# Optimization experiments

Hardware: AMD Instinct MI355X
Metric: run time of the kernel (lower is better)

Reference implementation:

```python
import jax, jax.numpy as jnp
import numpy as np

B, T, I, H, V = 32, 64, 512, 512, 32000


def setup_inputs() -> dict:
    key = jax.random.key(0)
    ks = jax.random.split(key, 8)
    s_in = 1.0 / np.sqrt(H)  # torch LSTMCell/Linear uniform init scale
    return {
        "isequence": jax.random.normal(ks[0], (B, T, I), dtype=jnp.float32),
        "hidden_t": jax.random.normal(ks[1], (B, H), dtype=jnp.float32),
        "W_ih": jax.random.uniform(ks[2], (4 * H, I), jnp.float32, -s_in, s_in),
        "W_hh": jax.random.uniform(ks[3], (4 * H, H), jnp.float32, -s_in, s_in),
        "b_ih": jax.random.uniform(ks[4], (4 * H,), jnp.float32, -s_in, s_in),
        "b_hh": jax.random.uniform(ks[5], (4 * H,), jnp.float32, -s_in, s_in),
        "W_out": jax.random.uniform(ks[6], (V, H), jnp.float32, -s_in, s_in),
        "b_out": jax.random.uniform(ks[7], (V,), jnp.float32, -s_in, s_in),
    }


def reference(isequence, hidden_t, W_ih, W_hh, b_ih, b_hh, W_out, b_out):
    # isequence: [B, T, I] -> time-major [T, B, I] (matches permute(1,0,2))
    xs = jnp.transpose(isequence, (1, 0, 2))
    # Precompute input-to-gate projections for all timesteps: [T, B, 4H]
    x_gates = jnp.einsum("tbi,gi->tbg", xs, W_ih) + b_ih + b_hh
    c0 = jnp.zeros_like(hidden_t)  # init_hidden zeros cell state

    def step(carry, xg):
        h, c = carry
        gates = xg + h @ W_hh.T  # [B, 4H], torch gate order: i, f, g, o
        i_g, f_g, g_g, o_g = jnp.split(gates, 4, axis=-1)
        i_g = jax.nn.sigmoid(i_g)
        f_g = jax.nn.sigmoid(f_g)
        g_g = jnp.tanh(g_g)
        o_g = jax.nn.sigmoid(o_g)
        c_new = f_g * c + i_g * g_g
        h_new = o_g * jnp.tanh(c_new)
        logits = h_new @ W_out.T + b_out  # [B, V]
        return (h_new, c_new), logits

    _, osequence = jax.lax.scan(step, (hidden_t, c0), x_gates)  # [T, B, V]
    return jnp.transpose(osequence, (1, 0, 2))  # [B, T, V]
```

## Files before the change

kernel.cpp:

```cpp
#include <hip/hip_runtime.h>
#include <hip/hip_bf16.h>

typedef unsigned short u16;
typedef unsigned int u32;
typedef __attribute__((ext_vector_type(4))) float f32x4;
typedef __attribute__((ext_vector_type(8))) short short8;
typedef __attribute__((ext_vector_type(4))) unsigned short u16x4;
typedef __attribute__((ext_vector_type(4))) unsigned int u32x4;

#define LSTM_NBLK 16

static __device__ __forceinline__ u16 f2bf(float f) {
  union { float f; unsigned u; } v; v.f = f;
  unsigned r = v.u + 0x7FFFu + ((v.u >> 16) & 1u);
  return (u16)(r >> 16);
}

static __device__ __forceinline__ void gload_lds16(const void* g, void* l) {
  __builtin_amdgcn_global_load_lds(
      (const __attribute__((address_space(1))) unsigned int*)g,
      (__attribute__((address_space(3))) unsigned int*)l, 16, 0, 0);
}

static __device__ __forceinline__ short8 ld_b128_sc(const void* p) {
  short8 r;
  asm volatile("global_load_dwordx4 %0, %1, off sc0 sc1"
               : "=v"(r) : "v"(p) : "memory");
  return r;
}
static __device__ __forceinline__ unsigned ld_u32_sc_wait(const unsigned* p) {
  unsigned r;
  asm volatile("global_load_dword %0, %1, off sc0 sc1\n\ts_waitcnt vmcnt(0)"
               : "=v"(r) : "v"(p) : "memory");
  return r;
}
static __device__ __forceinline__ void st_u32_sc(void* p, unsigned v) {
  asm volatile("global_store_dword %0, %1, off sc0 sc1"
               :: "v"(p), "v"(v) : "memory");
}
static __device__ __forceinline__ void waitcnt0() {
  asm volatile("s_waitcnt vmcnt(0)" ::: "memory");
  __builtin_amdgcn_sched_barrier(0);
}

__global__ void prep_kernel(const float* __restrict__ iseq, const float* __restrict__ h0,
                            const float* __restrict__ wih, const float* __restrict__ whh,
                            const float* __restrict__ wout,
                            u16* __restrict__ wout_bf, u16* __restrict__ wih_bf,
                            u16* __restrict__ whh_bf, u16* __restrict__ ax,
                            u32* __restrict__ h2u, unsigned* __restrict__ flags) {
  const int S0 = 4096000;
  const int S1 = S0 + 262144;
  const int S2 = S1 + 262144;
  const int S3 = S2 + 262144;
  const int S4 = S3 + 8192;
  const int S5 = S4 + 256;
  int u = blockIdx.x * blockDim.x + threadIdx.x;
  int stride = gridDim.x * blockDim.x;
  for (; u < S5; u += stride) {
    if (u < S0) {
      int e = u * 4; f32x4 v = *(const f32x4*)(wout + e);
      u16x4 o; o[0]=f2bf(v[0]); o[1]=f2bf(v[1]); o[2]=f2bf(v[2]); o[3]=f2bf(v[3]);
      *(u16x4*)(wout_bf + e) = o;
    } else if (u < S1) {
      int e = (u - S0) * 4; f32x4 v = *(const f32x4*)(wih + e);
      u16x4 o; o[0]=f2bf(v[0]); o[1]=f2bf(v[1]); o[2]=f2bf(v[2]); o[3]=f2bf(v[3]);
      *(u16x4*)(wih_bf + e) = o;
    } else if (u < S2) {
      int e = (u - S1) * 4; f32x4 v = *(const f32x4*)(whh + e);
      u16x4 o; o[0]=f2bf(v[0]); o[1]=f2bf(v[1]); o[2]=f2bf(v[2]); o[3]=f2bf(v[3]);
      *(u16x4*)(whh_bf + e) = o;
    } else if (u < S3) {
      int e = (u - S2) * 4; int m = e >> 9; int k = e & 511;
      int b = m & 31; int t = m >> 5;
      f32x4 v = *(const f32x4*)(iseq + ((b * 64 + t) << 9) + k);
      u16x4 o; o[0]=f2bf(v[0]); o[1]=f2bf(v[1]); o[2]=f2bf(v[2]); o[3]=f2bf(v[3]);
      *(u16x4*)(ax + e) = o;
    } else if (u < S4) {
      int v = u - S3;
      int e = v * 2;
      float lo = h0[e], hi = h0[e + 1];
      h2u[v] = (((u32)f2bf(hi)) << 16) | (u32)f2bf(lo);
    } else {
      flags[u - S4] = 0u;
    }
  }
}

__global__ __launch_bounds__(256, 2) void gemm_bt(
    const u16* __restrict__ A, const u16* __restrict__ Bw,
    float* __restrict__ C, const float* __restrict__ bias1,
    const float* __restrict__ bias2, int N, int remap) {
  __shared__ u16 As[2][8192];
  __shared__ u16 Bs[2][8192];
  const int tid = threadIdx.x;
  const int w = tid >> 6, l = tid & 63;
  const int wr = w >> 1, wc = w & 1;
  const int tm = blockIdx.y * 128, tn = blockIdx.x * 128;

  f32x4 acc[4][4];
#pragma unroll
  for (int i = 0; i < 4; ++i)
#pragma unroll
    for (int j = 0; j < 4; ++j) acc[i][j] = (f32x4){0.f, 0.f, 0.f, 0.f};

  auto stage = [&](int buf, int kt) {
#pragma unroll
    for (int i = 0; i < 4; ++i) {
      int r = (w * 4 + i) * 8 + (l >> 3);
      int c16 = (l & 7) ^ (r & 7);
      int rowm = tm + r;
      const u16* srca;
      if (remap) {
        srca = A + ((rowm & 63) + 1) * 16384 + (rowm >> 6) * 512 + kt * 64 + c16 * 8;
      } else {
        srca = A + rowm * 512 + kt * 64 + c16 * 8;
      }
      gload_lds16(srca, &As[buf][(w * 4 + i) * 512]);
      const u16* srcb = Bw + (tn + r) * 512 + kt * 64 + c16 * 8;
      gload_lds16(srcb, &Bs[buf][(w * 4 + i) * 512]);
    }
  };

  stage(0, 0);
  int buf = 0;
  for (int kt = 0; kt < 8; ++kt) {
    __syncthreads();
    if (kt < 7) stage(buf ^ 1, kt + 1);
#pragma unroll
    for (int kk = 0; kk < 2; ++kk) {
      short8 af[4], bfr[4];
#pragma unroll
      for (int mi = 0; mi < 4; ++mi) {
        int row = wr * 64 + mi * 16 + (l & 15);
        int s = (kk * 4 + (l >> 4)) ^ (row & 7);
        af[mi] = *(const short8*)&As[buf][row * 64 + s * 8];
      }
#pragma unroll
      for (int ni = 0; ni < 4; ++ni) {
        int row = wc * 64 + ni * 16 + (l & 15);
        int s = (kk * 4 + (l >> 4)) ^ (row & 7);
        bfr[ni] = *(const short8*)&Bs[buf][row * 64 + s * 8];
      }
#pragma unroll
      for (int mi = 0; mi < 4; ++mi)
#pragma unroll
        for (int ni = 0; ni < 4; ++ni)
          acc[mi][ni] = __builtin_amdgcn_mfma_f32_16x16x32_bf16(
              af[mi], bfr[ni], acc[mi][ni], 0, 0, 0);
    }
    buf ^= 1;
  }

#pragma unroll
  for (int ni = 0; ni < 4; ++ni) {
    int gcol = tn + wc * 64 + ni * 16 + (l & 15);
    float bv = 0.f;
    if (bias1) bv += bias1[gcol];
    if (bias2) bv += bias2[gcol];
#pragma unroll
    for (int mi = 0; mi < 4; ++mi) {
      int grow0 = tm + wr * 64 + mi * 16 + ((l >> 4) << 2);
      f32x4 a = acc[mi][ni];
#pragma unroll
      for (int q = 0; q < 4; ++q) {
        C[(long long)(grow0 + q) * N + gcol] = a[q] + bv;
      }
    }
  }
}

__global__ __launch_bounds__(512, 1) void lstm_persist(
    const u16* __restrict__ whh, const float* __restrict__ xg,
    u16* __restrict__ h2, unsigned* __restrict__ flags) {
  __shared__ u16 hbuf[32 * 512];
  __shared__ u16 hloc[1024];
  const int tid = threadIdx.x;
  const int w = tid >> 6, l = tid & 63;
  const int blk = blockIdx.x;
  const int j0 = (blk * 8 + w) * 4;
  const int c = l & 15;
  const int wrow = (c >> 2) * 512 + j0 + (c & 3);
  const int ko = (l >> 4) * 8;
  u32* h2u = (u32*)h2;

  short8 bfr[16];
  const u16* wp = whh + wrow * 512 + ko;
#pragma unroll
  for (int kt = 0; kt < 16; ++kt) bfr[kt] = *(const short8*)(wp + kt * 32);

  const int rq = (l >> 4) * 4;
  const int jj = l & 3;
  const int b0 = l & 15, b1 = 16 + (l & 15);
  const int s0 = b0 & 7;

  const int cb = tid & 31;
  const int ckg = tid >> 5;
  const int csw = cb & 7;

  const int ob = tid >> 4;
  const int oj = tid & 15;

  float creg[2][4];
#pragma unroll
  for (int mt = 0; mt < 2; ++mt)
#pragma unroll
    for (int q = 0; q < 4; ++q) creg[mt][q] = 0.f;

  float xcur[2][4], xnext[2][4];
#pragma unroll
  for (int mt = 0; mt < 2; ++mt)
#pragma unroll
    for (int q = 0; q < 4; ++q)
      xcur[mt][q] = xg[(mt * 16 + rq + q) * 2048 + wrow];

  for (int it = 0; it < 64; ++it) {
    if (it > 0 && w == 0) {
      const unsigned want = (unsigned)it;
      for (;;) {
        unsigned f = ld_u32_sc_wait(flags + blk * 16 + (l & 15));
        if (__all((int)(f >= want))) break;
      }
    }
    __syncthreads();

    {
      const u16* src = h2 + it * 16384 + cb * 512 + ckg * 32;
      short8 d0 = ld_b128_sc(src);
      short8 d1 = ld_b128_sc(src + 8);
      short8 d2 = ld_b128_sc(src + 16);
      short8 d3 = ld_b128_sc(src + 24);
      waitcnt0();
      *(short8*)&hbuf[cb * 512 + (((ckg * 4 + 0) ^ csw) * 8)] = d0;
      *(short8*)&hbuf[cb * 512 + (((ckg * 4 + 1) ^ csw) * 8)] = d1;
      *(short8*)&hbuf[cb * 512 + (((ckg * 4 + 2) ^ csw) * 8)] = d2;
      *(short8*)&hbuf[cb * 512 + (((ckg * 4 + 3) ^ csw) * 8)] = d3;
    }
    __syncthreads();

    f32x4 acc0 = (f32x4){0.f, 0.f, 0.f, 0.f};
    f32x4 acc1 = (f32x4){0.f, 0.f, 0.f, 0.f};
#pragma unroll
    for (int kt = 0; kt < 16; ++kt) {
      int x = ((kt * 4 + (l >> 4)) ^ s0) * 8;
      short8 a0 = *(const short8*)&hbuf[b0 * 512 + x];
      short8 a1 = *(const short8*)&hbuf[b1 * 512 + x];
      acc0 = __builtin_amdgcn_mfma_f32_16x16x32_bf16(a0, bfr[kt], acc0, 0, 0, 0);
      acc1 = __builtin_amdgcn_mfma_f32_16x16x32_bf16(a1, bfr[kt], acc1, 0, 0, 0);
    }
    if (it < 63) {
#pragma unroll
      for (int mt = 0; mt < 2; ++mt)
#pragma unroll
        for (int q = 0; q < 4; ++q)
          xnext[mt][q] = xg[((it + 1) * 32 + mt * 16 + rq + q) * 2048 + wrow];
    }

#pragma unroll
    for (int mt = 0; mt < 2; ++mt) {
#pragma unroll
      for (int q = 0; q < 4; ++q) {
        int b = mt * 16 + rq + q;
        float av = (mt == 0) ? acc0[q] : acc1[q];
        float gp = av + xcur[mt][q];
        int bl = (l & 48) | jj;
        float xi = __shfl(gp, bl);
        float xf = __shfl(gp, bl | 4);
        float xgg = __shfl(gp, bl | 8);
        float xo = __shfl(gp, bl | 12);
        float is = 1.f / (1.f + __expf(-xi));
        float fs = 1.f / (1.f + __expf(-xf));
        float e2 = __expf(2.f * xgg);
        float gt = 1.f - 2.f / (e2 + 1.f);
        float os = 1.f / (1.f + __expf(-xo));
        float cn = fs * creg[mt][q] + is * gt;
        creg[mt][q] = cn;
        float e2c = __expf(2.f * cn);
        float hn = os * (1.f - 2.f / (e2c + 1.f));
        if ((l & 12) == 0) {
          hloc[b * 32 + w * 4 + jj] = f2bf(hn);
        }
      }
    }
    __syncthreads();

    {
      u32 v = *(const u32*)&hloc[ob * 32 + oj * 2];
      st_u32_sc(h2u + (it + 1) * 8192 + ob * 256 + blk * 16 + oj, v);
      waitcnt0();
    }
    __syncthreads();

    if (it < 63) {
      if (w == 0 && l < 16)
        st_u32_sc(flags + l * 16 + blk, (unsigned)(it + 1));
#pragma unroll
      for (int mt = 0; mt < 2; ++mt)
#pragma unroll
        for (int q = 0; q < 4; ++q)
          xcur[mt][q] = xnext[mt][q];
    }
  }
}

extern "C" void kernel_launch(void* const* d_in, const int* in_sizes, int n_in,
                              void* d_out, int out_size, void* d_ws, size_t ws_size,
                              hipStream_t stream) {
  (void)in_sizes; (void)n_in; (void)out_size; (void)ws_size;
  const float* iseq = (const float*)d_in[0];
  const float* h0   = (const float*)d_in[1];
  const float* wih  = (const float*)d_in[2];
  const float* whh  = (const float*)d_in[3];
  const float* bih  = (const float*)d_in[4];
  const float* bhh  = (const float*)d_in[5];
  const float* wout = (const float*)d_in[6];
  const float* bout = (const float*)d_in[7];

  char* ws = (char*)d_ws;
  u16* wout_bf = (u16*)(ws + 0);
  u16* wih_bf  = (u16*)(ws + 32768000);
  u16* whh_bf  = (u16*)(ws + 34865152);
  u16* ax      = (u16*)(ws + 36962304);
  u16* h2      = (u16*)(ws + 39059456);
  unsigned* flags = (unsigned*)(ws + 41189376);
  float* xg    = (float*)(ws + 41254912);
  float* out   = (float*)d_out;

  prep_kernel<<<4096, 256, 0, stream>>>(iseq, h0, wih, whh, wout,
                                        wout_bf, wih_bf, whh_bf, ax,
                                        (u32*)h2, flags);
  gemm_bt<<<dim3(16, 16), 256, 0, stream>>>(ax, wih_bf, xg, bih, bhh, 2048, 0);
  lstm_persist<<<LSTM_NBLK, 512, 0, stream>>>(whh_bf, xg, h2, flags);
  gemm_bt<<<dim3(250, 16), 256, 0, stream>>>(h2, wout_bf, out, bout, nullptr, 32000, 1);
}
```

Before: 580.9 us.

## Replace flag-based LSTM step sync with tagged hidden-state words polled directly

The persistent LSTM kernel no longer publishes per-block flags and spins on them. Each bf16 hidden value is now stored in a 32-bit word with the step number in its upper half, and consumers poll the data itself until every tag matches. This removes a store-wait, a flag round trip and two barriers per timestep. The hidden buffer in shared memory is double-buffered, and each block reads its own slice from shared memory instead of global. The cost is twice the bytes in the exchanged hidden state and a larger zero-initialised tagged buffer in prep.

```diff
diff --git a/kernel.cpp b/kernel.cpp
--- a/kernel.cpp
+++ b/kernel.cpp
@@ -6,6 +6,7 @@
 typedef __attribute__((ext_vector_type(4))) float f32x4;
 typedef __attribute__((ext_vector_type(8))) short short8;
 typedef __attribute__((ext_vector_type(4))) unsigned short u16x4;
+typedef __attribute__((ext_vector_type(2))) unsigned int u32x2;
 typedef __attribute__((ext_vector_type(4))) unsigned int u32x4;
 
 #define LSTM_NBLK 16
@@ -22,20 +23,15 @@
       (__attribute__((address_space(3))) unsigned int*)l, 16, 0, 0);
 }
 
-static __device__ __forceinline__ short8 ld_b128_sc(const void* p) {
-  short8 r;
+static __device__ __forceinline__ u32x4 ld_b128u_sc(const u32* p) {
+  u32x4 r;
   asm volatile("global_load_dwordx4 %0, %1, off sc0 sc1"
                : "=v"(r) : "v"(p) : "memory");
   return r;
 }
-static __device__ __forceinline__ unsigned ld_u32_sc_wait(const unsigned* p) {
-  unsigned r;
-  asm volatile("global_load_dword %0, %1, off sc0 sc1\n\ts_waitcnt vmcnt(0)"
-               : "=v"(r) : "v"(p) : "memory");
-  return r;
-}
-static __device__ __forceinline__ void st_u32_sc(void* p, unsigned v) {
-  asm volatile("global_store_dword %0, %1, off sc0 sc1"
+static __device__ __forceinline__ void st_u64_sc(void* p, u32 lo, u32 hi) {
+  u32x2 v; v[0] = lo; v[1] = hi;
+  asm volatile("global_store_dwordx2 %0, %1, off sc0 sc1"
                :: "v"(p), "v"(v) : "memory");
 }
 static __device__ __forceinline__ void waitcnt0() {
@@ -48,16 +44,17 @@
                             const float* __restrict__ wout,
                             u16* __restrict__ wout_bf, u16* __restrict__ wih_bf,
                             u16* __restrict__ whh_bf, u16* __restrict__ ax,
-                            u32* __restrict__ h2u, unsigned* __restrict__ flags) {
+                            u32* __restrict__ htag, u32* __restrict__ h2u) {
   const int S0 = 4096000;
   const int S1 = S0 + 262144;
   const int S2 = S1 + 262144;
   const int S3 = S2 + 262144;
-  const int S4 = S3 + 8192;
-  const int S5 = S4 + 256;
+  const int S4 = S3 + 4096;
+  const int S5 = S4 + 258048;
+  const int S6 = S5 + 2048;
   int u = blockIdx.x * blockDim.x + threadIdx.x;
   int stride = gridDim.x * blockDim.x;
-  for (; u < S5; u += stride) {
+  for (; u < S6; u += stride) {
     if (u < S0) {
       int e = u * 4; f32x4 v = *(const f32x4*)(wout + e);
       u16x4 o; o[0]=f2bf(v[0]); o[1]=f2bf(v[1]); o[2]=f2bf(v[2]); o[3]=f2bf(v[3]);
@@ -77,12 +74,26 @@
       u16x4 o; o[0]=f2bf(v[0]); o[1]=f2bf(v[1]); o[2]=f2bf(v[2]); o[3]=f2bf(v[3]);
       *(u16x4*)(ax + e) = o;
     } else if (u < S4) {
-      int v = u - S3;
+      int e = (u - S3) * 4; f32x4 v = *(const f32x4*)(h0 + e);
+      u32x4 o;
+      o[0] = (1u << 16) | f2bf(v[0]); o[1] = (1u << 16) | f2bf(v[1]);
+      o[2] = (1u << 16) | f2bf(v[2]); o[3] = (1u << 16) | f2bf(v[3]);
+      *(u32x4*)(htag + e) = o;
+    } else if (u < S5) {
+      int e = (u - S4) * 4;
+      u32x4 z = {0u, 0u, 0u, 0u};
+      *(u32x4*)(htag + 16384 + e) = z;
+    } else {
+      int v = (u - S5) * 4;
       int e = v * 2;
-      float lo = h0[e], hi = h0[e + 1];
-      h2u[v] = (((u32)f2bf(hi)) << 16) | (u32)f2bf(lo);
-    } else {
-      flags[u - S4] = 0u;
+      f32x4 x0 = *(const f32x4*)(h0 + e);
+      f32x4 x1 = *(const f32x4*)(h0 + e + 4);
+      u32x4 o;
+      o[0] = (((u32)f2bf(x0[1])) << 16) | (u32)f2bf(x0[0]);
+      o[1] = (((u32)f2bf(x0[3])) << 16) | (u32)f2bf(x0[2]);
+      o[2] = (((u32)f2bf(x1[1])) << 16) | (u32)f2bf(x1[0]);
+      o[3] = (((u32)f2bf(x1[3])) << 16) | (u32)f2bf(x1[2]);
+      *(u32x4*)(h2u + v) = o;
     }
   }
 }
@@ -172,8 +183,8 @@
 
 __global__ __launch_bounds__(512, 1) void lstm_persist(
     const u16* __restrict__ whh, const float* __restrict__ xg,
-    u16* __restrict__ h2, unsigned* __restrict__ flags) {
-  __shared__ u16 hbuf[32 * 512];
+    u16* __restrict__ h2, u32* __restrict__ htag) {
+  __shared__ u16 hbuf[2][32 * 512];
   __shared__ u16 hloc[1024];
   const int tid = threadIdx.x;
   const int w = tid >> 6, l = tid & 63;
@@ -198,8 +209,8 @@
   const int ckg = tid >> 5;
   const int csw = cb & 7;
 
-  const int ob = tid >> 4;
-  const int oj = tid & 15;
+  const int pb = tid >> 4;
+  const int pj = tid & 15;
 
   float creg[2][4];
 #pragma unroll
@@ -215,27 +226,46 @@
       xcur[mt][q] = xg[(mt * 16 + rq + q) * 2048 + wrow];
 
   for (int it = 0; it < 64; ++it) {
-    if (it > 0 && w == 0) {
-      const unsigned want = (unsigned)it;
+    u16* hb = hbuf[it & 1];
+    short8 d0, d1, d2, d3;
+    if (it > 0 && ckg == blk) {
+      d0 = *(const short8*)&hloc[cb * 32 + 0];
+      d1 = *(const short8*)&hloc[cb * 32 + 8];
+      d2 = *(const short8*)&hloc[cb * 32 + 16];
+      d3 = *(const short8*)&hloc[cb * 32 + 24];
+    } else {
+      const u32* src = htag + it * 16384 + cb * 512 + ckg * 32;
+      const unsigned want = (unsigned)(it + 1);
+      u32x4 a0, a1, a2, a3, a4, a5, a6, a7;
       for (;;) {
-        unsigned f = ld_u32_sc_wait(flags + blk * 16 + (l & 15));
-        if (__all((int)(f >= want))) break;
-      }
-    }
-    __syncthreads();
-
-    {
-      const u16* src = h2 + it * 16384 + cb * 512 + ckg * 32;
-      short8 d0 = ld_b128_sc(src);
-      short8 d1 = ld_b128_sc(src + 8);
-      short8 d2 = ld_b128_sc(src + 16);
-      short8 d3 = ld_b128_sc(src + 24);
-      waitcnt0();
-      *(short8*)&hbuf[cb * 512 + (((ckg * 4 + 0) ^ csw) * 8)] = d0;
-      *(short8*)&hbuf[cb * 512 + (((ckg * 4 + 1) ^ csw) * 8)] = d1;
-      *(short8*)&hbuf[cb * 512 + (((ckg * 4 + 2) ^ csw) * 8)] = d2;
-      *(short8*)&hbuf[cb * 512 + (((ckg * 4 + 3) ^ csw) * 8)] = d3;
-    }
+        a0 = ld_b128u_sc(src +  0); a1 = ld_b128u_sc(src +  4);
+        a2 = ld_b128u_sc(src +  8); a3 = ld_b128u_sc(src + 12);
+        a4 = ld_b128u_sc(src + 16); a5 = ld_b128u_sc(src + 20);
+        a6 = ld_b128u_sc(src + 24); a7 = ld_b128u_sc(src + 28);
+        waitcnt0();
+        unsigned d = 0;
+#pragma unroll
+        for (int q2 = 0; q2 < 4; ++q2) {
+          d |= (a0[q2] >> 16) ^ want; d |= (a1[q2] >> 16) ^ want;
+          d |= (a2[q2] >> 16) ^ want; d |= (a3[q2] >> 16) ^ want;
+          d |= (a4[q2] >> 16) ^ want; d |= (a5[q2] >> 16) ^ want;
+          d |= (a6[q2] >> 16) ^ want; d |= (a7[q2] >> 16) ^ want;
+        }
+        if (d == 0) break;
+      }
+      d0[0]=(short)a0[0]; d0[1]=(short)a0[1]; d0[2]=(short)a0[2]; d0[3]=(short)a0[3];
+      d0[4]=(short)a1[0]; d0[5]=(short)a1[1]; d0[6]=(short)a1[2]; d0[7]=(short)a1[3];
+      d1[0]=(short)a2[0]; d1[1]=(short)a2[1]; d1[2]=(short)a2[2]; d1[3]=(short)a2[3];
+      d1[4]=(short)a3[0]; d1[5]=(short)a3[1]; d1[6]=(short)a3[2]; d1[7]=(short)a3[3];
+      d2[0]=(short)a4[0]; d2[1]=(short)a4[1]; d2[2]=(short)a4[2]; d2[3]=(short)a4[3];
+      d2[4]=(short)a5[0]; d2[5]=(short)a5[1]; d2[6]=(short)a5[2]; d2[7]=(short)a5[3];
+      d3[0]=(short)a6[0]; d3[1]=(short)a6[1]; d3[2]=(short)a6[2]; d3[3]=(short)a6[3];
+      d3[4]=(short)a7[0]; d3[5]=(short)a7[1]; d3[6]=(short)a7[2]; d3[7]=(short)a7[3];
+    }
+    *(short8*)&hb[cb * 512 + (((ckg * 4 + 0) ^ csw) * 8)] = d0;
+    *(short8*)&hb[cb * 512 + (((ckg * 4 + 1) ^ csw) * 8)] = d1;
+    *(short8*)&hb[cb * 512 + (((ckg * 4 + 2) ^ csw) * 8)] = d2;
+    *(short8*)&hb[cb * 512 + (((ckg * 4 + 3) ^ csw) * 8)] = d3;
     __syncthreads();
 
     f32x4 acc0 = (f32x4){0.f, 0.f, 0.f, 0.f};
@@ -243,8 +273,8 @@
 #pragma unroll
     for (int kt = 0; kt < 16; ++kt) {
       int x = ((kt * 4 + (l >> 4)) ^ s0) * 8;
-      short8 a0 = *(const short8*)&hbuf[b0 * 512 + x];
-      short8 a1 = *(const short8*)&hbuf[b1 * 512 + x];
+      short8 a0 = *(const short8*)&hb[b0 * 512 + x];
+      short8 a1 = *(const short8*)&hb[b1 * 512 + x];
       acc0 = __builtin_amdgcn_mfma_f32_16x16x32_bf16(a0, bfr[kt], acc0, 0, 0, 0);
       acc1 = __builtin_amdgcn_mfma_f32_16x16x32_bf16(a1, bfr[kt], acc1, 0, 0, 0);
     }
@@ -260,7 +290,6 @@
     for (int mt = 0; mt < 2; ++mt) {
 #pragma unroll
       for (int q = 0; q < 4; ++q) {
-        int b = mt * 16 + rq + q;
         float av = (mt == 0) ? acc0[q] : acc1[q];
         float gp = av + xcur[mt][q];
         int bl = (l & 48) | jj;
@@ -278,6 +307,7 @@
         float e2c = __expf(2.f * cn);
         float hn = os * (1.f - 2.f / (e2c + 1.f));
         if ((l & 12) == 0) {
+          int b = mt * 16 + rq + q;
           hloc[b * 32 + w * 4 + jj] = f2bf(hn);
         }
       }
@@ -285,15 +315,16 @@
     __syncthreads();
 
     {
-      u32 v = *(const u32*)&hloc[ob * 32 + oj * 2];
-      st_u32_sc(h2u + (it + 1) * 8192 + ob * 256 + blk * 16 + oj, v);
-      waitcnt0();
-    }
-    __syncthreads();
-
+      u32 lo = (u32)hloc[pb * 32 + pj * 2];
+      u32 hi = (u32)hloc[pb * 32 + pj * 2 + 1];
+      h2u[(it + 1) * 8192 + pb * 256 + blk * 16 + pj] = (hi << 16) | lo;
+      if (it < 63) {
+        u32 tag = ((u32)(it + 2)) << 16;
+        st_u64_sc(htag + (it + 1) * 16384 + pb * 512 + blk * 32 + pj * 2,
+                  tag | lo, tag | hi);
+      }
+    }
     if (it < 63) {
-      if (w == 0 && l < 16)
-        st_u32_sc(flags + l * 16 + blk, (unsigned)(it + 1));
 #pragma unroll
       for (int mt = 0; mt < 2; ++mt)
 #pragma unroll
@@ -322,14 +353,14 @@
   u16* whh_bf  = (u16*)(ws + 34865152);
   u16* ax      = (u16*)(ws + 36962304);
   u16* h2      = (u16*)(ws + 39059456);
-  unsigned* flags = (unsigned*)(ws + 41189376);
-  float* xg    = (float*)(ws + 41254912);
+  u32* htag    = (u32*)(ws + 41189376);
+  float* xg    = (float*)(ws + 45383680);
   float* out   = (float*)d_out;
 
   prep_kernel<<<4096, 256, 0, stream>>>(iseq, h0, wih, whh, wout,
                                         wout_bf, wih_bf, whh_bf, ax,
-                                        (u32*)h2, flags);
+                                        htag, (u32*)h2);
   gemm_bt<<<dim3(16, 16), 256, 0, stream>>>(ax, wih_bf, xg, bih, bhh, 2048, 0);
-  lstm_persist<<<LSTM_NBLK, 512, 0, stream>>>(whh_bf, xg, h2, flags);
+  lstm_persist<<<LSTM_NBLK, 512, 0, stream>>>(whh_bf, xg, h2, htag);
   gemm_bt<<<dim3(250, 16), 256, 0, stream>>>(h2, wout_bf, out, bout, nullptr, 32000, 1);
 }
```

New measurement: 649.7 us. 1.12x slower.
